# Optimization experiments

Measured on AMD Instinct MI355X. Metric: run time of the kernel, lower is better.

Reference implementation:

```python
import jax, jax.numpy as jnp
import numpy as np

N_NODES = 50000
N_EDGES = 800000
NDIM_IN = 64
EDIM = 32
HIDDEN = 128
NDIM_OUT = 64


def setup_inputs() -> dict:
    key = jax.random.key(0)
    ks = jax.random.split(key, 12)
    glorot = lambda k, fi, fo: jax.random.normal(k, (fi, fo), jnp.float32) * np.sqrt(2.0 / (fi + fo))
    return {
        "x": jax.random.normal(ks[0], (N_NODES, NDIM_IN), jnp.float32),
        "edge_index": jax.random.randint(ks[1], (2, N_EDGES), 0, N_NODES, jnp.int64),
        "edge_attr": jax.random.normal(ks[2], (N_EDGES, EDIM), jnp.float32),
        # layer 1: SAGELayer(ndim_in=64, edim=32, ndim_out=128)
        "W_msg1": glorot(ks[3], NDIM_IN + EDIM, HIDDEN),
        "b_msg1": jnp.zeros((HIDDEN,), jnp.float32),
        "W_app1": glorot(ks[4], NDIM_IN + HIDDEN, HIDDEN),
        "b_app1": jnp.zeros((HIDDEN,), jnp.float32),
        # layer 2: SAGELayer(ndim_in=128, edim=32, ndim_out=64)
        "W_msg2": glorot(ks[5], HIDDEN + EDIM, NDIM_OUT),
        "b_msg2": jnp.zeros((NDIM_OUT,), jnp.float32),
        "W_app2": glorot(ks[6], HIDDEN + NDIM_OUT, NDIM_OUT),
        "b_app2": jnp.zeros((NDIM_OUT,), jnp.float32),
    }


def _sage_layer(x, src, dst, edge_attr, W_msg, b_msg, W_app, b_app):
    # message: per-edge gather of source features, concat with edge attrs, linear
    msg = jnp.concatenate([x[src], edge_attr], axis=-1) @ W_msg + b_msg  # [E, d_out]
    # mean-scatter aggregate at destination nodes (0 for isolated nodes, as in PyG)
    n = x.shape[0]
    summed = jax.ops.segment_sum(msg, dst, num_segments=n)              # [N, d_out]
    cnt = jax.ops.segment_sum(jnp.ones((src.shape[0], 1), x.dtype), dst, num_segments=n)
    aggr = summed / jnp.maximum(cnt, 1.0)
    # update: concat self features with aggregate, linear, relu
    return jax.nn.relu(jnp.concatenate([x, aggr], axis=-1) @ W_app + b_app)


def reference(x, edge_index, edge_attr,
              W_msg1, b_msg1, W_app1, b_app1,
              W_msg2, b_msg2, W_app2, b_app2):
    src, dst = edge_index[0], edge_index[1]
    h = _sage_layer(x, src, dst, edge_attr, W_msg1, b_msg1, W_app1, b_app1)
    # dropout is identity in eval mode
    h = _sage_layer(h, src, dst, edge_attr, W_msg2, b_msg2, W_app2, b_app2)
    return h
```

## Files before the change

kernel.cpp:

```cpp
#include <hip/hip_runtime.h>

#define SCAN_CHUNK 1024
#define NPB 32

typedef unsigned int   uint32;
typedef unsigned short ushort16;
typedef __attribute__((ext_vector_type(8))) short bf16x8;
typedef __attribute__((ext_vector_type(4))) float f32x4;
#define MFMA16(a,b,c) __builtin_amdgcn_mfma_f32_16x16x32_bf16(a,b,c,0,0,0)

__device__ inline uint32 pack_bf16x2(float a, float b) {
    uint32 ua = __float_as_uint(a);
    uint32 ub = __float_as_uint(b);
    ua += 0x7FFFu + ((ua >> 16) & 1u);
    ub += 0x7FFFu + ((ub >> 16) & 1u);
    return (ua >> 16) | (ub & 0xFFFF0000u);
}
__device__ inline ushort16 bf16_1(float a) {
    uint32 u = __float_as_uint(a);
    u += 0x7FFFu + ((u >> 16) & 1u);
    return (ushort16)(u >> 16);
}
__device__ inline float bf_lo(uint32 u) { return __uint_as_float(u << 16); }
__device__ inline float bf_hi(uint32 u) { return __uint_as_float(u & 0xFFFF0000u); }

__global__ void zero_kernel(int4* __restrict__ p, int n4)
{
    int i = blockIdx.x * blockDim.x + threadIdx.x;
    if (i < n4) p[i] = make_int4(0, 0, 0, 0);
}

__global__ void cvt_x_kernel(const float4* __restrict__ xin,
                             uint2* __restrict__ xb, int n4)
{
    int i = blockIdx.x * blockDim.x + threadIdx.x;
    if (i < n4) {
        float4 v = xin[i];
        uint2 o;
        o.x = pack_bf16x2(v.x, v.y);
        o.y = pack_bf16x2(v.z, v.w);
        xb[i] = o;
    }
}

__global__ void hist_kernel(const int* __restrict__ dst, int* __restrict__ deg, int E)
{
    int g = blockIdx.x * blockDim.x + threadIdx.x;
    int e0 = g * 8;
    if (e0 + 8 <= E) {
        int4 da = *(const int4*)&dst[e0];
        int4 db = *(const int4*)&dst[e0 + 4];
        atomicAdd(&deg[da.x], 1);
        atomicAdd(&deg[da.y], 1);
        atomicAdd(&deg[da.z], 1);
        atomicAdd(&deg[da.w], 1);
        atomicAdd(&deg[db.x], 1);
        atomicAdd(&deg[db.y], 1);
        atomicAdd(&deg[db.z], 1);
        atomicAdd(&deg[db.w], 1);
    } else {
        for (int e = e0; e < E; e++) atomicAdd(&deg[dst[e]], 1);
    }
}

__global__ __launch_bounds__(256) void scanA_kernel(const int* __restrict__ deg,
                                                    int* __restrict__ part, int N)
{
    __shared__ int red[256];
    int b = blockIdx.x, t = threadIdx.x;
    int base = b * SCAN_CHUNK;
    int s = 0;
    for (int i = t; i < SCAN_CHUNK; i += 256) {
        int idx = base + i;
        s += (idx < N) ? deg[idx] : 0;
    }
    red[t] = s;
    __syncthreads();
    for (int o = 128; o > 0; o >>= 1) {
        if (t < o) red[t] += red[t + o];
        __syncthreads();
    }
    if (t == 0) part[b] = red[0];
}

__global__ void scanB_kernel(int* __restrict__ part, int* __restrict__ offN, int NCH)
{
    int lane = threadIdx.x;
    int orig = (lane < NCH) ? part[lane] : 0;
    int v = orig;
    for (int s = 1; s < 64; s <<= 1) {
        int t = __shfl_up(v, s);
        if (lane >= s) v += t;
    }
    if (lane < NCH) part[lane] = v - orig;
    if (lane == NCH - 1) *offN = v;
}

__global__ __launch_bounds__(SCAN_CHUNK) void scanC_kernel(const int* __restrict__ deg,
                                                           const int* __restrict__ part,
                                                           int* __restrict__ off,
                                                           int* __restrict__ cursor, int N)
{
    __shared__ int buf[SCAN_CHUNK];
    int b = blockIdx.x, t = threadIdx.x;
    int idx = b * SCAN_CHUNK + t;
    int v = (idx < N) ? deg[idx] : 0;
    buf[t] = v;
    __syncthreads();
    for (int s = 1; s < SCAN_CHUNK; s <<= 1) {
        int tmp = (t >= s) ? buf[t - s] : 0;
        __syncthreads();
        buf[t] += tmp;
        __syncthreads();
    }
    int excl = buf[t] - v + part[b];
    if (idx < N) { off[idx] = excl; cursor[idx] = excl; }
}

__global__ void fill_kernel(const int* __restrict__ src, const int* __restrict__ dst,
                            int* __restrict__ cursor, int2* __restrict__ elist, int E)
{
    int g = blockIdx.x * blockDim.x + threadIdx.x;
    int e0 = g * 8;
    if (e0 + 8 <= E) {
        int4 sa = *(const int4*)&src[e0];
        int4 sb = *(const int4*)&src[e0 + 4];
        int4 da = *(const int4*)&dst[e0];
        int4 db = *(const int4*)&dst[e0 + 4];
        int p0 = atomicAdd(&cursor[da.x], 1);
        int p1 = atomicAdd(&cursor[da.y], 1);
        int p2 = atomicAdd(&cursor[da.z], 1);
        int p3 = atomicAdd(&cursor[da.w], 1);
        int p4 = atomicAdd(&cursor[db.x], 1);
        int p5 = atomicAdd(&cursor[db.y], 1);
        int p6 = atomicAdd(&cursor[db.z], 1);
        int p7 = atomicAdd(&cursor[db.w], 1);
        elist[p0] = make_int2(sa.x, e0 + 0);
        elist[p1] = make_int2(sa.y, e0 + 1);
        elist[p2] = make_int2(sa.z, e0 + 2);
        elist[p3] = make_int2(sa.w, e0 + 3);
        elist[p4] = make_int2(sb.x, e0 + 4);
        elist[p5] = make_int2(sb.y, e0 + 5);
        elist[p6] = make_int2(sb.z, e0 + 6);
        elist[p7] = make_int2(sb.w, e0 + 7);
    } else {
        for (int e = e0; e < E; e++) {
            int p = atomicAdd(&cursor[dst[e]], 1);
            elist[p] = make_int2(src[e], e);
        }
    }
}

__global__ __launch_bounds__(128) void compose1_kernel(
    const float* __restrict__ Wmsg1, const float* __restrict__ bmsg1,
    const float* __restrict__ Wapp1, const float* __restrict__ bapp1,
    ushort16* __restrict__ Wc1T, float* __restrict__ b1eff, float* __restrict__ bmW1)
{
    int b = blockIdx.x;
    int j = threadIdx.x;
    if (b < 64) {
        Wc1T[(size_t)j * 160 + b] = bf16_1(Wapp1[b * 128 + j]);
    } else if (b < 160) {
        int ar = b - 64;
        float s = 0.f;
        for (int k = 0; k < 128; k++)
            s = fmaf(Wmsg1[ar * 128 + k], Wapp1[(64 + k) * 128 + j], s);
        Wc1T[(size_t)j * 160 + b] = bf16_1(s);
    } else {
        float s = 0.f;
        for (int k = 0; k < 128; k++)
            s = fmaf(bmsg1[k], Wapp1[(64 + k) * 128 + j], s);
        bmW1[j] = s;
        b1eff[j] = bapp1[j] + s;
    }
}

__global__ __launch_bounds__(64) void compose2_kernel(
    const float* __restrict__ Wmsg2, const float* __restrict__ bmsg2,
    const float* __restrict__ Wapp2, const float* __restrict__ bapp2,
    ushort16* __restrict__ Wc2T, float* __restrict__ b2eff, float* __restrict__ bmW2)
{
    int b = blockIdx.x;
    int j = threadIdx.x;
    if (b < 192) {
        Wc2T[(size_t)j * 224 + b] = bf16_1(Wapp2[b * 64 + j]);
    } else if (b < 224) {
        int ar = 128 + (b - 192);
        float s = 0.f;
        for (int k = 0; k < 64; k++)
            s = fmaf(Wmsg2[ar * 64 + k], Wapp2[(128 + k) * 64 + j], s);
        Wc2T[(size_t)j * 224 + b] = bf16_1(s);
    } else {
        float s = 0.f;
        for (int k = 0; k < 64; k++)
            s = fmaf(bmsg2[k], Wapp2[(128 + k) * 64 + j], s);
        bmW2[j] = s;
        b2eff[j] = bapp2[j] + s;
    }
}

__global__ __launch_bounds__(64) void composem_kernel(
    const float* __restrict__ Wmsg2, ushort16* __restrict__ Wm2hT)
{
    int k = blockIdx.x;
    int c = threadIdx.x;
    Wm2hT[(size_t)c * 128 + k] = bf16_1(Wmsg2[k * 64 + c]);
}

__global__ __launch_bounds__(256) void agg1_kernel(const uint4* __restrict__ xb,
                                                   const float4* __restrict__ ea4,
                                                   const int2* __restrict__ elist,
                                                   const int* __restrict__ off,
                                                   float4* __restrict__ A1x,
                                                   float4* __restrict__ A1e, int N)
{
    int tid = blockIdx.x * blockDim.x + threadIdx.x;
    int node = tid >> 3;
    int s8 = tid & 7;
    if (node >= N) return;
    int beg = off[node], end = off[node + 1];
    float inv = 1.0f / fmaxf((float)(end - beg), 1.0f);

    float ax[8];
#pragma unroll
    for (int q = 0; q < 8; q++) ax[q] = 0.f;
    float4 ae = make_float4(0.f, 0.f, 0.f, 0.f);

    int i = beg;
    for (; i + 4 <= end; i += 4) {
        int2 p0 = elist[i + 0];
        int2 p1 = elist[i + 1];
        int2 p2 = elist[i + 2];
        int2 p3 = elist[i + 3];
        uint4 vx0 = xb[(size_t)p0.x * 8 + s8];
        uint4 vx1 = xb[(size_t)p1.x * 8 + s8];
        uint4 vx2 = xb[(size_t)p2.x * 8 + s8];
        uint4 vx3 = xb[(size_t)p3.x * 8 + s8];
        float4 ve0 = ea4[(size_t)p0.y * 8 + s8];
        float4 ve1 = ea4[(size_t)p1.y * 8 + s8];
        float4 ve2 = ea4[(size_t)p2.y * 8 + s8];
        float4 ve3 = ea4[(size_t)p3.y * 8 + s8];
        ax[0] += (bf_lo(vx0.x) + bf_lo(vx1.x)) + (bf_lo(vx2.x) + bf_lo(vx3.x));
        ax[1] += (bf_hi(vx0.x) + bf_hi(vx1.x)) + (bf_hi(vx2.x) + bf_hi(vx3.x));
        ax[2] += (bf_lo(vx0.y) + bf_lo(vx1.y)) + (bf_lo(vx2.y) + bf_lo(vx3.y));
        ax[3] += (bf_hi(vx0.y) + bf_hi(vx1.y)) + (bf_hi(vx2.y) + bf_hi(vx3.y));
        ax[4] += (bf_lo(vx0.z) + bf_lo(vx1.z)) + (bf_lo(vx2.z) + bf_lo(vx3.z));
        ax[5] += (bf_hi(vx0.z) + bf_hi(vx1.z)) + (bf_hi(vx2.z) + bf_hi(vx3.z));
        ax[6] += (bf_lo(vx0.w) + bf_lo(vx1.w)) + (bf_lo(vx2.w) + bf_lo(vx3.w));
        ax[7] += (bf_hi(vx0.w) + bf_hi(vx1.w)) + (bf_hi(vx2.w) + bf_hi(vx3.w));
        ae.x += (ve0.x + ve1.x) + (ve2.x + ve3.x);
        ae.y += (ve0.y + ve1.y) + (ve2.y + ve3.y);
        ae.z += (ve0.z + ve1.z) + (ve2.z + ve3.z);
        ae.w += (ve0.w + ve1.w) + (ve2.w + ve3.w);
    }
    for (; i < end; i++) {
        int2 pr = elist[i];
        uint4 vx = xb[(size_t)pr.x * 8 + s8];
        float4 ve = ea4[(size_t)pr.y * 8 + s8];
        ax[0] += bf_lo(vx.x); ax[1] += bf_hi(vx.x);
        ax[2] += bf_lo(vx.y); ax[3] += bf_hi(vx.y);
        ax[4] += bf_lo(vx.z); ax[5] += bf_hi(vx.z);
        ax[6] += bf_lo(vx.w); ax[7] += bf_hi(vx.w);
        ae.x += ve.x; ae.y += ve.y; ae.z += ve.z; ae.w += ve.w;
    }
    float4 o0 = make_float4(ax[0] * inv, ax[1] * inv, ax[2] * inv, ax[3] * inv);
    float4 o1 = make_float4(ax[4] * inv, ax[5] * inv, ax[6] * inv, ax[7] * inv);
    A1x[(size_t)node * 16 + s8 * 2 + 0] = o0;
    A1x[(size_t)node * 16 + s8 * 2 + 1] = o1;
    ae.x *= inv; ae.y *= inv; ae.z *= inv; ae.w *= inv;
    A1e[(size_t)node * 8 + s8] = ae;
}

__global__ __launch_bounds__(256) void agg2_kernel(const uint4* __restrict__ g2b,
                                                   const int2* __restrict__ elist,
                                                   const int* __restrict__ off,
                                                   float4* __restrict__ A2g, int N)
{
    int tid = blockIdx.x * blockDim.x + threadIdx.x;
    int node = tid >> 3;
    int s8 = tid & 7;
    if (node >= N) return;
    int beg = off[node], end = off[node + 1];
    float inv = 1.0f / fmaxf((float)(end - beg), 1.0f);

    float ag[8];
#pragma unroll
    for (int q = 0; q < 8; q++) ag[q] = 0.f;

    int i = beg;
    for (; i + 4 <= end; i += 4) {
        int r0 = elist[i + 0].x;
        int r1 = elist[i + 1].x;
        int r2 = elist[i + 2].x;
        int r3 = elist[i + 3].x;
        uint4 v0 = g2b[(size_t)r0 * 8 + s8];
        uint4 v1 = g2b[(size_t)r1 * 8 + s8];
        uint4 v2 = g2b[(size_t)r2 * 8 + s8];
        uint4 v3 = g2b[(size_t)r3 * 8 + s8];
        ag[0] += (bf_lo(v0.x) + bf_lo(v1.x)) + (bf_lo(v2.x) + bf_lo(v3.x));
        ag[1] += (bf_hi(v0.x) + bf_hi(v1.x)) + (bf_hi(v2.x) + bf_hi(v3.x));
        ag[2] += (bf_lo(v0.y) + bf_lo(v1.y)) + (bf_lo(v2.y) + bf_lo(v3.y));
        ag[3] += (bf_hi(v0.y) + bf_hi(v1.y)) + (bf_hi(v2.y) + bf_hi(v3.y));
        ag[4] += (bf_lo(v0.z) + bf_lo(v1.z)) + (bf_lo(v2.z) + bf_lo(v3.z));
        ag[5] += (bf_hi(v0.z) + bf_hi(v1.z)) + (bf_hi(v2.z) + bf_hi(v3.z));
        ag[6] += (bf_lo(v0.w) + bf_lo(v1.w)) + (bf_lo(v2.w) + bf_lo(v3.w));
        ag[7] += (bf_hi(v0.w) + bf_hi(v1.w)) + (bf_hi(v2.w) + bf_hi(v3.w));
    }
    for (; i < end; i++) {
        int row = elist[i].x;
        uint4 v = g2b[(size_t)row * 8 + s8];
        ag[0] += bf_lo(v.x); ag[1] += bf_hi(v.x);
        ag[2] += bf_lo(v.y); ag[3] += bf_hi(v.y);
        ag[4] += bf_lo(v.z); ag[5] += bf_hi(v.z);
        ag[6] += bf_lo(v.w); ag[7] += bf_hi(v.w);
    }
    float4 o0 = make_float4(ag[0] * inv, ag[1] * inv, ag[2] * inv, ag[3] * inv);
    float4 o1 = make_float4(ag[4] * inv, ag[5] * inv, ag[6] * inv, ag[7] * inv);
    A2g[(size_t)node * 16 + s8 * 2 + 0] = o0;
    A2g[(size_t)node * 16 + s8 * 2 + 1] = o1;
}

__global__ __launch_bounds__(512) void node1_kernel(
    const uint32* __restrict__ xb,
    const float* __restrict__ A1x,
    const float* __restrict__ A1e,
    const int*   __restrict__ deg,
    const ushort16* __restrict__ Wc1T,
    const float* __restrict__ b1eff,
    const float* __restrict__ bmW1,
    const ushort16* __restrict__ Wm2hT,
    uint32* __restrict__ h1b,
    uint32* __restrict__ g2b,
    int N)
{
    __shared__ ushort16 sFb[NPB][168];
    __shared__ ushort16 sHb[NPB][168];
    __shared__ float sCnt[NPB];

    int t = threadIdx.x;
    int base = blockIdx.x * NPB;
    int tr = t >> 4, c16 = t & 15;
    int v = base + tr;
    bool vok = v < N;

    uint32* sFrow = (uint32*)&sFb[tr][0];
#pragma unroll
    for (int m = 0; m < 5; m++) {
        int d = c16 + 16 * m;
        uint32 w = 0;
        if (vok) {
            if (d < 32) {
                w = xb[(size_t)v * 32 + d];
            } else if (d < 64) {
                int o = (d - 32) * 2;
                w = pack_bf16x2(A1x[(size_t)v * 64 + o], A1x[(size_t)v * 64 + o + 1]);
            } else {
                int o = (d - 64) * 2;
                w = pack_bf16x2(A1e[(size_t)v * 32 + o], A1e[(size_t)v * 32 + o + 1]);
            }
        }
        sFrow[d] = w;
    }
    if (t < NPB) sCnt[t] = (base + t < N) ? (float)deg[base + t] : 1.f;
    __syncthreads();

    int lane = t & 63;
    int wv = t >> 6;
    int lr = lane & 15;
    int kg = lane >> 4;

    f32x4 acc0 = {0.f, 0.f, 0.f, 0.f};
    f32x4 acc1 = {0.f, 0.f, 0.f, 0.f};
    const ushort16* bp1 = &Wc1T[(size_t)(wv * 16 + lr) * 160 + kg * 8];
#pragma unroll
    for (int kt = 0; kt < 5; kt++) {
        bf16x8 a0 = *(const bf16x8*)&sFb[lr][kt * 32 + kg * 8];
        bf16x8 a1 = *(const bf16x8*)&sFb[16 + lr][kt * 32 + kg * 8];
        bf16x8 b  = *(const bf16x8*)&bp1[kt * 32];
        acc0 = MFMA16(a0, b, acc0);
        acc1 = MFMA16(a1, b, acc1);
    }
    int col = wv * 16 + lr;
    float bj = b1eff[col], bw = bmW1[col];
#pragma unroll
    for (int rt = 0; rt < 2; rt++) {
        f32x4 acc = rt ? acc1 : acc0;
        int r0 = rt * 16 + kg * 4;
#pragma unroll
        for (int reg = 0; reg < 4; reg++) {
            float c = sCnt[r0 + reg];
            float hv = fmaxf(acc[reg] + (c > 0.f ? bj : bj - bw), 0.f);
            float other = __shfl_xor(hv, 1);
            if (!(lane & 1))
                ((uint32*)&sHb[r0 + reg][0])[col >> 1] = pack_bf16x2(hv, other);
        }
    }
    __syncthreads();

#pragma unroll
    for (int m = 0; m < 4; m++) {
        int d = c16 + 16 * m;
        if (vok) h1b[(size_t)v * 64 + d] = ((uint32*)&sHb[tr][0])[d];
    }

    int rt2 = wv >> 2, ct2 = wv & 3;
    f32x4 accg = {0.f, 0.f, 0.f, 0.f};
    const ushort16* bp2 = &Wm2hT[(size_t)(ct2 * 16 + lr) * 128 + kg * 8];
#pragma unroll
    for (int kt = 0; kt < 4; kt++) {
        bf16x8 a = *(const bf16x8*)&sHb[rt2 * 16 + lr][kt * 32 + kg * 8];
        bf16x8 b = *(const bf16x8*)&bp2[kt * 32];
        accg = MFMA16(a, b, accg);
    }
    int colg = ct2 * 16 + lr;
    int rg0 = rt2 * 16 + kg * 4;
#pragma unroll
    for (int reg = 0; reg < 4; reg++) {
        float other = __shfl_xor(accg[reg], 1);
        int vr = base + rg0 + reg;
        if (!(lane & 1) && vr < N)
            g2b[(size_t)vr * 32 + (colg >> 1)] = pack_bf16x2(accg[reg], other);
    }
}

__global__ __launch_bounds__(512) void node2_kernel(
    const uint32* __restrict__ h1b,
    const float* __restrict__ A2g,
    const float* __restrict__ A1e,
    const int*   __restrict__ deg,
    const ushort16* __restrict__ Wc2T,
    const float* __restrict__ b2eff,
    const float* __restrict__ bmW2,
    float* __restrict__ out,
    int N)
{
    __shared__ ushort16 sFb[NPB][232];
    __shared__ float sCnt[NPB];

    int t = threadIdx.x;
    int base = blockIdx.x * NPB;
    int tr = t >> 4, c16 = t & 15;
    int v = base + tr;
    bool vok = v < N;

    uint32* sFrow = (uint32*)&sFb[tr][0];
#pragma unroll
    for (int m = 0; m < 7; m++) {
        int d = c16 + 16 * m;
        uint32 w = 0;
        if (vok) {
            if (d < 64) {
                w = h1b[(size_t)v * 64 + d];
            } else if (d < 96) {
                int o = (d - 64) * 2;
                w = pack_bf16x2(A2g[(size_t)v * 64 + o], A2g[(size_t)v * 64 + o + 1]);
            } else {
                int o = (d - 96) * 2;
                w = pack_bf16x2(A1e[(size_t)v * 32 + o], A1e[(size_t)v * 32 + o + 1]);
            }
        }
        sFrow[d] = w;
    }
    if (t < NPB) sCnt[t] = (base + t < N) ? (float)deg[base + t] : 1.f;
    __syncthreads();

    int lane = t & 63;
    int wv = t >> 6;
    int lr = lane & 15;
    int kg = lane >> 4;
    int rt = wv >> 2, ct = wv & 3;

    f32x4 acc = {0.f, 0.f, 0.f, 0.f};
    const ushort16* bp = &Wc2T[(size_t)(ct * 16 + lr) * 224 + kg * 8];
#pragma unroll
    for (int kt = 0; kt < 7; kt++) {
        bf16x8 a = *(const bf16x8*)&sFb[rt * 16 + lr][kt * 32 + kg * 8];
        bf16x8 b = *(const bf16x8*)&bp[kt * 32];
        acc = MFMA16(a, b, acc);
    }
    int col = ct * 16 + lr;
    float bj = b2eff[col], bw = bmW2[col];
    int r0 = rt * 16 + kg * 4;
#pragma unroll
    for (int reg = 0; reg < 4; reg++) {
        int vr = base + r0 + reg;
        float c = sCnt[r0 + reg];
        float bias = (c > 0.f) ? bj : bj - bw;
        if (vr < N) out[(size_t)vr * 64 + col] = fmaxf(acc[reg] + bias, 0.f);
    }
}

extern "C" void kernel_launch(void* const* d_in, const int* in_sizes, int n_in,
                              void* d_out, int out_size, void* d_ws, size_t ws_size,
                              hipStream_t stream) {
    const float* x      = (const float*)d_in[0];
    const int*   ei     = (const int*)d_in[1];
    const float* ea     = (const float*)d_in[2];
    const float* Wmsg1  = (const float*)d_in[3];
    const float* bmsg1  = (const float*)d_in[4];
    const float* Wapp1  = (const float*)d_in[5];
    const float* bapp1  = (const float*)d_in[6];
    const float* Wmsg2  = (const float*)d_in[7];
    const float* bmsg2  = (const float*)d_in[8];
    const float* Wapp2  = (const float*)d_in[9];
    const float* bapp2  = (const float*)d_in[10];

    const int N = in_sizes[0] / 64;
    const int E = in_sizes[1] / 2;
    const int NCH = (N + SCAN_CHUNK - 1) / SCAN_CHUNK;
    const int* src = ei;
    const int* dst = ei + E;

    uint8_t* p = (uint8_t*)d_ws;
    auto alloc = [&](size_t bytes) -> void* {
        void* r = (void*)p;
        p += (bytes + 255) & ~(size_t)255;
        return r;
    };
    int*     deg    = (int*)alloc((size_t)(N + 3) / 4 * 16);
    int*     off    = (int*)alloc((size_t)(N + 1) * 4);
    int*     cursor = (int*)alloc((size_t)N * 4);
    int*     part   = (int*)alloc((size_t)NCH * 4);
    int2*    elist  = (int2*)alloc((size_t)E * 8);
    float*   A1x    = (float*)alloc((size_t)N * 64 * 4);
    float*   A1e    = (float*)alloc((size_t)N * 32 * 4);
    uint32*  xb     = (uint32*)alloc((size_t)N * 32 * 4);
    uint32*  h1b    = (uint32*)alloc((size_t)N * 64 * 4);
    uint32*  g2b    = (uint32*)alloc((size_t)N * 32 * 4);
    ushort16* Wc1T  = (ushort16*)alloc(128 * 160 * 2);
    ushort16* Wc2T  = (ushort16*)alloc(64 * 224 * 2);
    ushort16* Wm2hT = (ushort16*)alloc(64 * 128 * 2);
    float*   b1eff  = (float*)alloc(128 * 4);
    float*   bmW1   = (float*)alloc(128 * 4);
    float*   b2eff  = (float*)alloc(64 * 4);
    float*   bmW2   = (float*)alloc(64 * 4);
    float*   A2g    = A1x;

    {
        int n4 = (N + 3) / 4;
        zero_kernel<<<(n4 + 255) / 256, 256, 0, stream>>>((int4*)deg, n4);
    }

    compose1_kernel<<<161, 128, 0, stream>>>(Wmsg1, bmsg1, Wapp1, bapp1,
                                             Wc1T, b1eff, bmW1);
    compose2_kernel<<<225, 64, 0, stream>>>(Wmsg2, bmsg2, Wapp2, bapp2,
                                            Wc2T, b2eff, bmW2);
    composem_kernel<<<128, 64, 0, stream>>>(Wmsg2, Wm2hT);
    {
        int n4 = N * 16;
        cvt_x_kernel<<<(n4 + 255) / 256, 256, 0, stream>>>(
            (const float4*)x, (uint2*)xb, n4);
    }

    {
        int ngroups = (E + 7) / 8;
        hist_kernel<<<(ngroups + 255) / 256, 256, 0, stream>>>(dst, deg, E);
        scanA_kernel<<<NCH, 256, 0, stream>>>(deg, part, N);
        scanB_kernel<<<1, 64, 0, stream>>>(part, off + N, NCH);
        scanC_kernel<<<NCH, SCAN_CHUNK, 0, stream>>>(deg, part, off, cursor, N);
        fill_kernel<<<(ngroups + 255) / 256, 256, 0, stream>>>(src, dst, cursor, elist, E);
    }

    agg1_kernel<<<(N + 31) / 32, 256, 0, stream>>>(
        (const uint4*)xb, (const float4*)ea, elist, off,
        (float4*)A1x, (float4*)A1e, N);
    node1_kernel<<<(N + NPB - 1) / NPB, 512, 0, stream>>>(
        xb, A1x, A1e, deg, Wc1T, b1eff, bmW1, Wm2hT, h1b, g2b, N);

    agg2_kernel<<<(N + 31) / 32, 256, 0, stream>>>(
        (const uint4*)g2b, elist, off, (float4*)A2g, N);
    node2_kernel<<<(N + NPB - 1) / NPB, 512, 0, stream>>>(
        h1b, A2g, A1e, deg, Wc2T, b2eff, bmW2,
        (float*)d_out, N);
}
```

Baseline: 197.6 us.

## Sort nodes by in-degree to balance aggregation wavefront work

Adds a degree histogram, a prefix scan over bins and a scatter that builds a permutation grouping nodes of equal in-degree. The agg1 and agg2 kernels then process nodes in permuted order, so lanes in a wavefront loop over similar edge counts and divergence from uneven degrees drops. In exchange there are two extra small kernels, global atomics on only 256 bins (heavily contended), and a loss of spatial locality in the node output writes and offset reads.

Result: slower. 441.2 us (+123.3%).

```diff
diff --git a/kernel.cpp b/kernel.cpp
--- a/kernel.cpp
+++ b/kernel.cpp
@@ -2,6 +2,7 @@
 
 #define SCAN_CHUNK 1024
 #define NPB 32
+#define NBINS 256
 
 typedef unsigned int   uint32;
 typedef unsigned short ushort16;
@@ -99,7 +100,8 @@
 __global__ __launch_bounds__(SCAN_CHUNK) void scanC_kernel(const int* __restrict__ deg,
                                                            const int* __restrict__ part,
                                                            int* __restrict__ off,
-                                                           int* __restrict__ cursor, int N)
+                                                           int* __restrict__ cursor,
+                                                           int* __restrict__ bhist, int N)
 {
     __shared__ int buf[SCAN_CHUNK];
     int b = blockIdx.x, t = threadIdx.x;
@@ -114,7 +116,38 @@
         __syncthreads();
     }
     int excl = buf[t] - v + part[b];
-    if (idx < N) { off[idx] = excl; cursor[idx] = excl; }
+    if (idx < N) {
+        off[idx] = excl; cursor[idx] = excl;
+        atomicAdd(&bhist[min(v, NBINS - 1)], 1);
+    }
+}
+
+__global__ __launch_bounds__(NBINS) void dscan_kernel(const int* __restrict__ bhist,
+                                                      int* __restrict__ bcursor)
+{
+    __shared__ int buf[NBINS];
+    int t = threadIdx.x;
+    int v = bhist[t];
+    buf[t] = v;
+    __syncthreads();
+    for (int s = 1; s < NBINS; s <<= 1) {
+        int tmp = (t >= s) ? buf[t - s] : 0;
+        __syncthreads();
+        buf[t] += tmp;
+        __syncthreads();
+    }
+    bcursor[t] = buf[t] - v;
+}
+
+__global__ void dscatter_kernel(const int* __restrict__ deg, int* __restrict__ bcursor,
+                                int* __restrict__ perm, int N)
+{
+    int i = blockIdx.x * blockDim.x + threadIdx.x;
+    if (i < N) {
+        int bin = min(deg[i], NBINS - 1);
+        int p = atomicAdd(&bcursor[bin], 1);
+        perm[p] = i;
+    }
 }
 
 __global__ void fill_kernel(const int* __restrict__ src, const int* __restrict__ dst,
@@ -211,13 +244,15 @@
                                                    const float4* __restrict__ ea4,
                                                    const int2* __restrict__ elist,
                                                    const int* __restrict__ off,
+                                                   const int* __restrict__ perm,
                                                    float4* __restrict__ A1x,
                                                    float4* __restrict__ A1e, int N)
 {
     int tid = blockIdx.x * blockDim.x + threadIdx.x;
-    int node = tid >> 3;
+    int gidx = tid >> 3;
     int s8 = tid & 7;
-    if (node >= N) return;
+    if (gidx >= N) return;
+    int node = perm[gidx];
     int beg = off[node], end = off[node + 1];
     float inv = 1.0f / fmaxf((float)(end - beg), 1.0f);
 
@@ -274,12 +309,14 @@
 __global__ __launch_bounds__(256) void agg2_kernel(const uint4* __restrict__ g2b,
                                                    const int2* __restrict__ elist,
                                                    const int* __restrict__ off,
+                                                   const int* __restrict__ perm,
                                                    float4* __restrict__ A2g, int N)
 {
     int tid = blockIdx.x * blockDim.x + threadIdx.x;
-    int node = tid >> 3;
+    int gidx = tid >> 3;
     int s8 = tid & 7;
-    if (node >= N) return;
+    if (gidx >= N) return;
+    int node = perm[gidx];
     int beg = off[node], end = off[node + 1];
     float inv = 1.0f / fmaxf((float)(end - beg), 1.0f);
 
@@ -517,10 +554,14 @@
         p += (bytes + 255) & ~(size_t)255;
         return r;
     };
-    int*     deg    = (int*)alloc((size_t)(N + 3) / 4 * 16);
+    int Npad = ((N + 3) / 4) * 4;
+    int*     deg    = (int*)alloc((size_t)Npad * 4 + NBINS * 4);
+    int*     bhist  = deg + Npad;
     int*     off    = (int*)alloc((size_t)(N + 1) * 4);
     int*     cursor = (int*)alloc((size_t)N * 4);
     int*     part   = (int*)alloc((size_t)NCH * 4);
+    int*     bcursor= (int*)alloc(NBINS * 4);
+    int*     perm   = (int*)alloc((size_t)N * 4);
     int2*    elist  = (int2*)alloc((size_t)E * 8);
     float*   A1x    = (float*)alloc((size_t)N * 64 * 4);
     float*   A1e    = (float*)alloc((size_t)N * 32 * 4);
@@ -537,7 +578,7 @@
     float*   A2g    = A1x;
 
     {
-        int n4 = (N + 3) / 4;
+        int n4 = Npad / 4 + NBINS / 4;
         zero_kernel<<<(n4 + 255) / 256, 256, 0, stream>>>((int4*)deg, n4);
     }
 
@@ -557,18 +598,20 @@
         hist_kernel<<<(ngroups + 255) / 256, 256, 0, stream>>>(dst, deg, E);
         scanA_kernel<<<NCH, 256, 0, stream>>>(deg, part, N);
         scanB_kernel<<<1, 64, 0, stream>>>(part, off + N, NCH);
-        scanC_kernel<<<NCH, SCAN_CHUNK, 0, stream>>>(deg, part, off, cursor, N);
+        scanC_kernel<<<NCH, SCAN_CHUNK, 0, stream>>>(deg, part, off, cursor, bhist, N);
+        dscan_kernel<<<1, NBINS, 0, stream>>>(bhist, bcursor);
+        dscatter_kernel<<<(N + 255) / 256, 256, 0, stream>>>(deg, bcursor, perm, N);
         fill_kernel<<<(ngroups + 255) / 256, 256, 0, stream>>>(src, dst, cursor, elist, E);
     }
 
     agg1_kernel<<<(N + 31) / 32, 256, 0, stream>>>(
-        (const uint4*)xb, (const float4*)ea, elist, off,
+        (const uint4*)xb, (const float4*)ea, elist, off, perm,
         (float4*)A1x, (float4*)A1e, N);
     node1_kernel<<<(N + NPB - 1) / NPB, 512, 0, stream>>>(
         xb, A1x, A1e, deg, Wc1T, b1eff, bmW1, Wm2hT, h1b, g2b, N);
 
     agg2_kernel<<<(N + 31) / 32, 256, 0, stream>>>(
-        (const uint4*)g2b, elist, off, (float4*)A2g, N);
+        (const uint4*)g2b, elist, off, perm, (float4*)A2g, N);
     node2_kernel<<<(N + NPB - 1) / NPB, 512, 0, stream>>>(
         h1b, A2g, A1e, deg, Wc2T, b2eff, bmW2,
         (float*)d_out, N);
```
